# Kernel tuning notes

Hardware: AMD Instinct MI355X
Metric: run time of the kernel (lower is better)

## Reference

```python
import jax, jax.numpy as jnp
import numpy as np

B, D, H = 65536, 64, 512  # batch, input_dim (even), hidden_dim; num_layers=4 -> 4 Linears


def setup_inputs() -> dict:
    key = jax.random.key(0)
    ks = jax.random.split(key, 10)
    s_in = 1.0 / np.sqrt(D)
    s_h = 1.0 / np.sqrt(H)
    return {
        "t": jnp.zeros((1,), jnp.float32),
        "x": jax.random.normal(ks[0], (B, D), jnp.float32),
        "W0": jax.random.uniform(ks[1], (D, H), jnp.float32, -s_in, s_in),
        "b0": jax.random.uniform(ks[2], (H,), jnp.float32, -s_in, s_in),
        "W1": jax.random.uniform(ks[3], (H, H), jnp.float32, -s_h, s_h),
        "b1": jax.random.uniform(ks[4], (H,), jnp.float32, -s_h, s_h),
        "W2": jax.random.uniform(ks[5], (H, H), jnp.float32, -s_h, s_h),
        "b2": jax.random.uniform(ks[6], (H,), jnp.float32, -s_h, s_h),
        "W3": jax.random.uniform(ks[7], (H, 1), jnp.float32, -s_h, s_h),
        "b3": jax.random.uniform(ks[8], (1,), jnp.float32, -s_h, s_h),
    }


def reference(t, x, W0, b0, W1, b1, W2, b2, W3, b3):
    # Hamiltonian MLP: Linear->Tanh x3, final Linear to scalar energy per sample.
    def hamiltonian_sum(xx):
        h = jnp.tanh(xx @ W0 + b0)
        h = jnp.tanh(h @ W1 + b1)
        h = jnp.tanh(h @ W2 + b2)
        return jnp.sum(h @ W3 + b3)

    gradH = jax.grad(hamiltonian_sum)(x)  # [B, D]
    n = D // 2
    # gradH @ J.T with symplectic J == concat(gradH_p, -gradH_q)
    return jnp.concatenate([gradH[:, n:], -gradH[:, :n]], axis=1)
```

## Files before the change

### kernel.cpp

```cpp
#include <hip/hip_runtime.h>
#include <hip/hip_bf16.h>

typedef unsigned short u16;
typedef short s16x8 __attribute__((ext_vector_type(8)));
typedef float f32x4 __attribute__((ext_vector_type(4)));

#define MFMA_BF16(a, b, c) __builtin_amdgcn_mfma_f32_16x16x32_bf16((a), (b), (c), 0, 0, 0)

static constexpr int D_IN   = 64;
static constexpr int H_DIM  = 512;
static constexpr int M_TILE = 64;
static constexpr int AST    = 520;
static constexpr int XST    = 72;

__device__ __forceinline__ u16 f2bf(float f) {
  unsigned u = __builtin_bit_cast(unsigned, f);
  u += 0x7fffu + ((u >> 16) & 1u);
  return (u16)(u >> 16);
}
__device__ __forceinline__ float bfb2f(unsigned bits16) {
  return __builtin_bit_cast(float, bits16 << 16);
}
__device__ __forceinline__ float fast_tanh(float x) {
  float e = __expf(2.0f * x);
  return 1.0f - 2.0f * __builtin_amdgcn_rcpf(e + 1.0f);
}

__global__ void prep_weights(const float* __restrict__ W0,
                             const float* __restrict__ W1,
                             const float* __restrict__ W2,
                             u16* __restrict__ ws) {
  u16* p0f = ws;
  u16* p0b = p0f + D_IN * H_DIM;
  u16* p1f = p0b + D_IN * H_DIM;
  u16* p1b = p1f + H_DIM * H_DIM;
  u16* p2f = p1b + H_DIM * H_DIM;
  u16* p2b = p2f + H_DIM * H_DIM;

  int t = blockIdx.x * 256 + threadIdx.x;
  int lane = t & 63;
  int kc   = (t >> 6) & 15;
  int ntg  = t >> 10;
  int ln = lane & 15, q = lane >> 4;
  int n = ntg * 16 + ln;
  int k = kc * 32 + q * 8;

  #pragma unroll
  for (int j = 0; j < 8; ++j) {
    p1f[t * 8 + j] = f2bf(W1[(k + j) * 512 + n]);
    p2f[t * 8 + j] = f2bf(W2[(k + j) * 512 + n]);
    p1b[t * 8 + j] = f2bf(W1[n * 512 + (k + j)]);
    p2b[t * 8 + j] = f2bf(W2[n * 512 + (k + j)]);
  }
  if (kc < 2) {
    int t0 = (ntg * 2 + kc) * 64 + lane;
    #pragma unroll
    for (int j = 0; j < 8; ++j)
      p0f[t0 * 8 + j] = f2bf(W0[(k + j) * 512 + n]);
  }
  if (ntg < 4) {
    int t0 = (ntg * 16 + kc) * 64 + lane;
    #pragma unroll
    for (int j = 0; j < 8; ++j)
      p0b[t0 * 8 + j] = f2bf(W0[n * 512 + (k + j)]);
  }
}

#define LOAD_B4(BP, KC, BB)                                                     \
  {                                                                             \
    const u16* _sr = (BP) + ((size_t)wave << 15) + ((KC) << 9) + lane * 8;      \
    _Pragma("unroll")                                                           \
    for (int s = 0; s < 4; ++s)                                                 \
      (BB)[s] = *(const s16x8*)(_sr + (s << 13));                               \
  }
#define BB_PROLOGUE3(BP)                                                        \
  { LOAD_B4(BP, 0, bb0); LOAD_B4(BP, 1, bb1); LOAD_B4(BP, 2, bb2); }

#define STEP3(KC, BB, BP)                                                       \
  {                                                                             \
    s16x8 a[4];                                                                 \
    _Pragma("unroll")                                                           \
    for (int mt = 0; mt < 4; ++mt)                                              \
      a[mt] = *(const s16x8*)(buf + (mt * 16 + ln) * AST + (KC) * 32 + q * 8);  \
    _Pragma("unroll")                                                           \
    for (int nt = 0; nt < 4; ++nt)                                              \
      _Pragma("unroll")                                                         \
      for (int mt = 0; mt < 4; ++mt)                                            \
        acc[mt][nt] = MFMA_BF16(a[mt], (BB)[nt], acc[mt][nt]);                  \
    if ((KC) + 3 < 16) LOAD_B4(BP, (KC) + 3, BB);                               \
  }

#define GEMM512_REG(BP)                                                         \
  {                                                                             \
    _Pragma("unroll") for (int mt = 0; mt < 4; ++mt)                            \
      _Pragma("unroll") for (int nt = 0; nt < 4; ++nt)                          \
        acc[mt][nt] = (f32x4){0.f, 0.f, 0.f, 0.f};                              \
    STEP3( 0, bb0, BP); STEP3( 1, bb1, BP); STEP3( 2, bb2, BP);                 \
    STEP3( 3, bb0, BP); STEP3( 4, bb1, BP); STEP3( 5, bb2, BP);                 \
    STEP3( 6, bb0, BP); STEP3( 7, bb1, BP); STEP3( 8, bb2, BP);                 \
    STEP3( 9, bb0, BP); STEP3(10, bb1, BP); STEP3(11, bb2, BP);                 \
    STEP3(12, bb0, BP); STEP3(13, bb1, BP); STEP3(14, bb2, BP);                 \
    STEP3(15, bb0, BP);                                                         \
  }

__global__ __launch_bounds__(512, 2) void hnn_fused(
    const float* __restrict__ x,
    const float* __restrict__ bias0,
    const float* __restrict__ bias1,
    const float* __restrict__ bias2,
    const float* __restrict__ W3,
    const u16* __restrict__ ws,
    float* __restrict__ out)
{
  const u16* p0f = ws;
  const u16* p0b = p0f + D_IN * H_DIM;
  const u16* p1f = p0b + D_IN * H_DIM;
  const u16* p1b = p1f + H_DIM * H_DIM;
  const u16* p2f = p1b + H_DIM * H_DIM;
  const u16* p2b = p2f + H_DIM * H_DIM;

  __shared__ __align__(16) u16 xs[M_TILE * XST];
  __shared__ __align__(16) u16 buf[M_TILE * AST];

  const int tid  = threadIdx.x;
  const int wave = tid >> 6;
  const int lane = tid & 63;
  const int ln   = lane & 15;
  const int q    = lane >> 4;
  const int nwb  = wave * 64;
  const int row0 = blockIdx.x * M_TILE;

  {
    int r = tid >> 3, c = (tid & 7) * 8;
    const float4* src = (const float4*)(x + (size_t)(row0 + r) * D_IN + c);
    float4 f0 = src[0];
    float4 f1 = src[1];
    u16* dst = xs + r * XST + c;
    dst[0] = f2bf(f0.x); dst[1] = f2bf(f0.y); dst[2] = f2bf(f0.z); dst[3] = f2bf(f0.w);
    dst[4] = f2bf(f1.x); dst[5] = f2bf(f1.y); dst[6] = f2bf(f1.z); dst[7] = f2bf(f1.w);
  }
  __syncthreads();

  f32x4 acc[4][4];
  s16x8 bb0[4], bb1[4], bb2[4];
  unsigned h0p[4][4][2];
  unsigned h1p[4][4][2];
  float bias[4];

  #pragma unroll
  for (int nt = 0; nt < 4; ++nt) bias[nt] = bias0[nwb + nt * 16 + ln];
  #pragma unroll
  for (int mt = 0; mt < 4; ++mt)
    #pragma unroll
    for (int nt = 0; nt < 4; ++nt) acc[mt][nt] = (f32x4){0.f, 0.f, 0.f, 0.f};
  {
    const u16* bpw0 = p0f + (wave << 12) + lane * 8;
    #pragma unroll
    for (int kc = 0; kc < 2; ++kc) {
      s16x8 a0[4];
      #pragma unroll
      for (int mt = 0; mt < 4; ++mt)
        a0[mt] = *(const s16x8*)(xs + (mt * 16 + ln) * XST + kc * 32 + q * 8);
      #pragma unroll
      for (int nt = 0; nt < 4; ++nt) {
        s16x8 b = *(const s16x8*)(bpw0 + (nt << 10) + (kc << 9));
        #pragma unroll
        for (int mt = 0; mt < 4; ++mt)
          acc[mt][nt] = MFMA_BF16(a0[mt], b, acc[mt][nt]);
      }
    }
  }
  BB_PROLOGUE3(p1f);
  #pragma unroll
  for (int mt = 0; mt < 4; ++mt)
    #pragma unroll
    for (int nt = 0; nt < 4; ++nt) {
      int col = nwb + nt * 16 + ln;
      u16 u[4];
      #pragma unroll
      for (int r = 0; r < 4; ++r) {
        float th = fast_tanh(acc[mt][nt][r] + bias[nt]);
        u[r] = f2bf(th);
        buf[(mt * 16 + q * 4 + r) * AST + col] = u[r];
      }
      h0p[mt][nt][0] = (unsigned)u[0] | ((unsigned)u[1] << 16);
      h0p[mt][nt][1] = (unsigned)u[2] | ((unsigned)u[3] << 16);
    }
  __syncthreads();

  #pragma unroll
  for (int nt = 0; nt < 4; ++nt) bias[nt] = bias1[nwb + nt * 16 + ln];
  GEMM512_REG(p1f);
  __syncthreads();
  BB_PROLOGUE3(p2f);
  #pragma unroll
  for (int mt = 0; mt < 4; ++mt)
    #pragma unroll
    for (int nt = 0; nt < 4; ++nt) {
      int col = nwb + nt * 16 + ln;
      u16 u[4];
      #pragma unroll
      for (int r = 0; r < 4; ++r) {
        float th = fast_tanh(acc[mt][nt][r] + bias[nt]);
        u[r] = f2bf(th);
        buf[(mt * 16 + q * 4 + r) * AST + col] = u[r];
      }
      h1p[mt][nt][0] = (unsigned)u[0] | ((unsigned)u[1] << 16);
      h1p[mt][nt][1] = (unsigned)u[2] | ((unsigned)u[3] << 16);
    }
  __syncthreads();

  #pragma unroll
  for (int nt = 0; nt < 4; ++nt) bias[nt] = bias2[nwb + nt * 16 + ln];
  float w3v[4];
  #pragma unroll
  for (int nt = 0; nt < 4; ++nt) w3v[nt] = W3[nwb + nt * 16 + ln];
  GEMM512_REG(p2f);
  __syncthreads();
  BB_PROLOGUE3(p2b);
  #pragma unroll
  for (int mt = 0; mt < 4; ++mt)
    #pragma unroll
    for (int nt = 0; nt < 4; ++nt) {
      int col = nwb + nt * 16 + ln;
      #pragma unroll
      for (int r = 0; r < 4; ++r) {
        float th = fast_tanh(acc[mt][nt][r] + bias[nt]);
        float gz = w3v[nt] * (1.0f - th * th);
        buf[(mt * 16 + q * 4 + r) * AST + col] = f2bf(gz);
      }
    }
  __syncthreads();

  GEMM512_REG(p2b);
  __syncthreads();
  BB_PROLOGUE3(p1b);
  #pragma unroll
  for (int mt = 0; mt < 4; ++mt)
    #pragma unroll
    for (int nt = 0; nt < 4; ++nt) {
      int col = nwb + nt * 16 + ln;
      unsigned pa = h1p[mt][nt][0], pb = h1p[mt][nt][1];
      float hh[4] = { bfb2f(pa & 0xffffu), bfb2f(pa >> 16),
                      bfb2f(pb & 0xffffu), bfb2f(pb >> 16) };
      #pragma unroll
      for (int r = 0; r < 4; ++r) {
        float gz = acc[mt][nt][r] * (1.0f - hh[r] * hh[r]);
        buf[(mt * 16 + q * 4 + r) * AST + col] = f2bf(gz);
      }
    }
  __syncthreads();

  GEMM512_REG(p1b);
  __syncthreads();
  #pragma unroll
  for (int mt = 0; mt < 4; ++mt)
    #pragma unroll
    for (int nt = 0; nt < 4; ++nt) {
      int col = nwb + nt * 16 + ln;
      unsigned pa = h0p[mt][nt][0], pb = h0p[mt][nt][1];
      float hh[4] = { bfb2f(pa & 0xffffu), bfb2f(pa >> 16),
                      bfb2f(pb & 0xffffu), bfb2f(pb >> 16) };
      #pragma unroll
      for (int r = 0; r < 4; ++r) {
        float gz = acc[mt][nt][r] * (1.0f - hh[r] * hh[r]);
        buf[(mt * 16 + q * 4 + r) * AST + col] = f2bf(gz);
      }
    }
  __syncthreads();

  {
    f32x4 acc5[2];
    acc5[0] = (f32x4){0.f, 0.f, 0.f, 0.f};
    acc5[1] = (f32x4){0.f, 0.f, 0.f, 0.f};
    const int mt5 = wave & 3;
    const int nb5 = (wave >> 2) * 32;
    const u16* bp5 = p0b + ((wave >> 2) << 14) + lane * 8;
    #pragma unroll 2
    for (int kc = 0; kc < 16; ++kc) {
      s16x8 a5 = *(const s16x8*)(buf + (mt5 * 16 + ln) * AST + kc * 32 + q * 8);
      #pragma unroll
      for (int nt = 0; nt < 2; ++nt) {
        s16x8 b = *(const s16x8*)(bp5 + (nt << 13) + (kc << 9));
        acc5[nt] = MFMA_BF16(a5, b, acc5[nt]);
      }
    }
    #pragma unroll
    for (int nt = 0; nt < 2; ++nt) {
      int g = nb5 + nt * 16 + ln;
      int c = (g < 32) ? g + 32 : g - 32;
      float s = (g < 32) ? -1.0f : 1.0f;
      #pragma unroll
      for (int r = 0; r < 4; ++r) {
        int grow = row0 + mt5 * 16 + q * 4 + r;
        out[(size_t)grow * 64 + c] = s * acc5[nt][r];
      }
    }
  }
}

extern "C" void kernel_launch(void* const* d_in, const int* in_sizes, int n_in,
                              void* d_out, int out_size, void* d_ws, size_t ws_size,
                              hipStream_t stream) {
  const float* x  = (const float*)d_in[1];
  const float* W0 = (const float*)d_in[2];
  const float* b0 = (const float*)d_in[3];
  const float* W1 = (const float*)d_in[4];
  const float* b1 = (const float*)d_in[5];
  const float* W2 = (const float*)d_in[6];
  const float* b2 = (const float*)d_in[7];
  const float* W3 = (const float*)d_in[8];
  u16* ws = (u16*)d_ws;
  float* out = (float*)d_out;

  prep_weights<<<128, 256, 0, stream>>>(W0, W1, W2, ws);
  hnn_fused<<<65536 / M_TILE, 512, 0, stream>>>(x, b0, b1, b2, W3, ws, out);
}
```

Before: 228.6 us.

## Transpose GEMM roles so weights are A operand, activations stored transposed

Swaps operand roles so each GEMM computes the transposed product (weights as the A operand in registers, activations read from LDS as B). Epilogues then write packed 4-element bf16 vectors instead of scalar u16 stores. Bias is folded into the accumulator init, W3 is folded into the backward W2 weights during prep, packed bf16 conversion is used on gfx950, and output is written as float4. The aim is to cut epilogue ALU work and the number of LDS and global store instructions, at the cost of a different LDS access pattern that may bank-conflict.

Result: slower. 264.0 us (+15.5%).

```diff
diff --git a/kernel.cpp b/kernel.cpp
--- a/kernel.cpp
+++ b/kernel.cpp
@@ -25,10 +25,22 @@
   float e = __expf(2.0f * x);
   return 1.0f - 2.0f * __builtin_amdgcn_rcpf(e + 1.0f);
 }
+#if defined(__gfx950__) && __has_builtin(__builtin_amdgcn_cvt_pk_bf16_f32)
+__device__ __forceinline__ unsigned pk2bf(float a, float b) {
+  typedef __bf16 bf16x2_t __attribute__((ext_vector_type(2)));
+  bf16x2_t v = __builtin_amdgcn_cvt_pk_bf16_f32(a, b);
+  return __builtin_bit_cast(unsigned, v);
+}
+#else
+__device__ __forceinline__ unsigned pk2bf(float a, float b) {
+  return (unsigned)f2bf(a) | ((unsigned)f2bf(b) << 16);
+}
+#endif
 
 __global__ void prep_weights(const float* __restrict__ W0,
                              const float* __restrict__ W1,
                              const float* __restrict__ W2,
+                             const float* __restrict__ W3,
                              u16* __restrict__ ws) {
   u16* p0f = ws;
   u16* p0b = p0f + D_IN * H_DIM;
@@ -50,7 +62,7 @@
     p1f[t * 8 + j] = f2bf(W1[(k + j) * 512 + n]);
     p2f[t * 8 + j] = f2bf(W2[(k + j) * 512 + n]);
     p1b[t * 8 + j] = f2bf(W1[n * 512 + (k + j)]);
-    p2b[t * 8 + j] = f2bf(W2[n * 512 + (k + j)]);
+    p2b[t * 8 + j] = f2bf(W2[n * 512 + (k + j)] * W3[k + j]);
   }
   if (kc < 2) {
     int t0 = (ntg * 2 + kc) * 64 + lane;
@@ -66,41 +78,55 @@
   }
 }
 
-#define LOAD_B4(BP, KC, BB)                                                     \
+#define LOAD_W4(BP, KC, WA)                                                     \
   {                                                                             \
     const u16* _sr = (BP) + ((size_t)wave << 15) + ((KC) << 9) + lane * 8;      \
     _Pragma("unroll")                                                           \
     for (int s = 0; s < 4; ++s)                                                 \
-      (BB)[s] = *(const s16x8*)(_sr + (s << 13));                               \
-  }
-#define BB_PROLOGUE3(BP)                                                        \
-  { LOAD_B4(BP, 0, bb0); LOAD_B4(BP, 1, bb1); LOAD_B4(BP, 2, bb2); }
-
-#define STEP3(KC, BB, BP)                                                       \
-  {                                                                             \
-    s16x8 a[4];                                                                 \
+      (WA)[s] = *(const s16x8*)(_sr + (s << 13));                               \
+  }
+#define WA_PROLOGUE3(BP)                                                        \
+  { LOAD_W4(BP, 0, wa0); LOAD_W4(BP, 1, wa1); LOAD_W4(BP, 2, wa2); }
+
+#define STEP3(KC, WA, BP)                                                       \
+  {                                                                             \
+    s16x8 b[4];                                                                 \
     _Pragma("unroll")                                                           \
-    for (int mt = 0; mt < 4; ++mt)                                              \
-      a[mt] = *(const s16x8*)(buf + (mt * 16 + ln) * AST + (KC) * 32 + q * 8);  \
+    for (int nt = 0; nt < 4; ++nt)                                              \
+      b[nt] = *(const s16x8*)(buf + (nt * 16 + ln) * AST + (KC) * 32 + q * 8);  \
     _Pragma("unroll")                                                           \
     for (int nt = 0; nt < 4; ++nt)                                              \
       _Pragma("unroll")                                                         \
       for (int mt = 0; mt < 4; ++mt)                                            \
-        acc[mt][nt] = MFMA_BF16(a[mt], (BB)[nt], acc[mt][nt]);                  \
-    if ((KC) + 3 < 16) LOAD_B4(BP, (KC) + 3, BB);                               \
+        acc[mt][nt] = MFMA_BF16((WA)[mt], b[nt], acc[mt][nt]);                  \
+    if ((KC) + 3 < 16) LOAD_W4(BP, (KC) + 3, WA);                               \
   }
 
 #define GEMM512_REG(BP)                                                         \
+  {                                                                             \
+    STEP3( 0, wa0, BP); STEP3( 1, wa1, BP); STEP3( 2, wa2, BP);                 \
+    STEP3( 3, wa0, BP); STEP3( 4, wa1, BP); STEP3( 5, wa2, BP);                 \
+    STEP3( 6, wa0, BP); STEP3( 7, wa1, BP); STEP3( 8, wa2, BP);                 \
+    STEP3( 9, wa0, BP); STEP3(10, wa1, BP); STEP3(11, wa2, BP);                 \
+    STEP3(12, wa0, BP); STEP3(13, wa1, BP); STEP3(14, wa2, BP);                 \
+    STEP3(15, wa0, BP);                                                         \
+  }
+
+#define ACC_INIT_BIAS(BIAS)                                                     \
+  {                                                                             \
+    _Pragma("unroll")                                                           \
+    for (int mt = 0; mt < 4; ++mt) {                                            \
+      float4 bv = *(const float4*)((BIAS) + wave * 64 + mt * 16 + q * 4);       \
+      _Pragma("unroll")                                                         \
+      for (int nt = 0; nt < 4; ++nt)                                            \
+        acc[mt][nt] = (f32x4){bv.x, bv.y, bv.z, bv.w};                          \
+    }                                                                           \
+  }
+#define ACC_INIT_ZERO()                                                         \
   {                                                                             \
     _Pragma("unroll") for (int mt = 0; mt < 4; ++mt)                            \
       _Pragma("unroll") for (int nt = 0; nt < 4; ++nt)                          \
         acc[mt][nt] = (f32x4){0.f, 0.f, 0.f, 0.f};                              \
-    STEP3( 0, bb0, BP); STEP3( 1, bb1, BP); STEP3( 2, bb2, BP);                 \
-    STEP3( 3, bb0, BP); STEP3( 4, bb1, BP); STEP3( 5, bb2, BP);                 \
-    STEP3( 6, bb0, BP); STEP3( 7, bb1, BP); STEP3( 8, bb2, BP);                 \
-    STEP3( 9, bb0, BP); STEP3(10, bb1, BP); STEP3(11, bb2, BP);                 \
-    STEP3(12, bb0, BP); STEP3(13, bb1, BP); STEP3(14, bb2, BP);                 \
-    STEP3(15, bb0, BP);                                                         \
   }
 
 __global__ __launch_bounds__(512, 2) void hnn_fused(
@@ -108,7 +134,6 @@
     const float* __restrict__ bias0,
     const float* __restrict__ bias1,
     const float* __restrict__ bias2,
-    const float* __restrict__ W3,
     const u16* __restrict__ ws,
     float* __restrict__ out)
 {
@@ -127,7 +152,7 @@
   const int lane = tid & 63;
   const int ln   = lane & 15;
   const int q    = lane >> 4;
-  const int nwb  = wave * 64;
+  const int m0   = wave * 64;
   const int row0 = blockIdx.x * M_TILE;
 
   {
@@ -142,130 +167,110 @@
   __syncthreads();
 
   f32x4 acc[4][4];
-  s16x8 bb0[4], bb1[4], bb2[4];
+  s16x8 wa0[4], wa1[4], wa2[4];
   unsigned h0p[4][4][2];
   unsigned h1p[4][4][2];
-  float bias[4];
-
-  #pragma unroll
-  for (int nt = 0; nt < 4; ++nt) bias[nt] = bias0[nwb + nt * 16 + ln];
-  #pragma unroll
-  for (int mt = 0; mt < 4; ++mt)
-    #pragma unroll
-    for (int nt = 0; nt < 4; ++nt) acc[mt][nt] = (f32x4){0.f, 0.f, 0.f, 0.f};
+
+  ACC_INIT_BIAS(bias0);
   {
-    const u16* bpw0 = p0f + (wave << 12) + lane * 8;
+    const u16* ap0 = p0f + (wave << 12) + lane * 8;
     #pragma unroll
     for (int kc = 0; kc < 2; ++kc) {
-      s16x8 a0[4];
+      s16x8 b[4];
       #pragma unroll
-      for (int mt = 0; mt < 4; ++mt)
-        a0[mt] = *(const s16x8*)(xs + (mt * 16 + ln) * XST + kc * 32 + q * 8);
+      for (int nt = 0; nt < 4; ++nt)
+        b[nt] = *(const s16x8*)(xs + (nt * 16 + ln) * XST + kc * 32 + q * 8);
       #pragma unroll
-      for (int nt = 0; nt < 4; ++nt) {
-        s16x8 b = *(const s16x8*)(bpw0 + (nt << 10) + (kc << 9));
+      for (int mt = 0; mt < 4; ++mt) {
+        s16x8 a = *(const s16x8*)(ap0 + (mt << 10) + (kc << 9));
         #pragma unroll
-        for (int mt = 0; mt < 4; ++mt)
-          acc[mt][nt] = MFMA_BF16(a0[mt], b, acc[mt][nt]);
+        for (int nt = 0; nt < 4; ++nt)
+          acc[mt][nt] = MFMA_BF16(a, b[nt], acc[mt][nt]);
       }
     }
   }
-  BB_PROLOGUE3(p1f);
-  #pragma unroll
-  for (int mt = 0; mt < 4; ++mt)
-    #pragma unroll
-    for (int nt = 0; nt < 4; ++nt) {
-      int col = nwb + nt * 16 + ln;
-      u16 u[4];
-      #pragma unroll
-      for (int r = 0; r < 4; ++r) {
-        float th = fast_tanh(acc[mt][nt][r] + bias[nt]);
-        u[r] = f2bf(th);
-        buf[(mt * 16 + q * 4 + r) * AST + col] = u[r];
-      }
-      h0p[mt][nt][0] = (unsigned)u[0] | ((unsigned)u[1] << 16);
-      h0p[mt][nt][1] = (unsigned)u[2] | ((unsigned)u[3] << 16);
-    }
-  __syncthreads();
-
-  #pragma unroll
-  for (int nt = 0; nt < 4; ++nt) bias[nt] = bias1[nwb + nt * 16 + ln];
+  WA_PROLOGUE3(p1f);
+  #pragma unroll
+  for (int mt = 0; mt < 4; ++mt)
+    #pragma unroll
+    for (int nt = 0; nt < 4; ++nt) {
+      unsigned p01 = pk2bf(fast_tanh(acc[mt][nt][0]), fast_tanh(acc[mt][nt][1]));
+      unsigned p23 = pk2bf(fast_tanh(acc[mt][nt][2]), fast_tanh(acc[mt][nt][3]));
+      h0p[mt][nt][0] = p01; h0p[mt][nt][1] = p23;
+      *(uint2*)(buf + (nt * 16 + ln) * AST + m0 + mt * 16 + q * 4) =
+          make_uint2(p01, p23);
+    }
+  __syncthreads();
+
+  ACC_INIT_BIAS(bias1);
   GEMM512_REG(p1f);
   __syncthreads();
-  BB_PROLOGUE3(p2f);
-  #pragma unroll
-  for (int mt = 0; mt < 4; ++mt)
-    #pragma unroll
-    for (int nt = 0; nt < 4; ++nt) {
-      int col = nwb + nt * 16 + ln;
-      u16 u[4];
-      #pragma unroll
-      for (int r = 0; r < 4; ++r) {
-        float th = fast_tanh(acc[mt][nt][r] + bias[nt]);
-        u[r] = f2bf(th);
-        buf[(mt * 16 + q * 4 + r) * AST + col] = u[r];
-      }
-      h1p[mt][nt][0] = (unsigned)u[0] | ((unsigned)u[1] << 16);
-      h1p[mt][nt][1] = (unsigned)u[2] | ((unsigned)u[3] << 16);
-    }
-  __syncthreads();
-
-  #pragma unroll
-  for (int nt = 0; nt < 4; ++nt) bias[nt] = bias2[nwb + nt * 16 + ln];
-  float w3v[4];
-  #pragma unroll
-  for (int nt = 0; nt < 4; ++nt) w3v[nt] = W3[nwb + nt * 16 + ln];
+  WA_PROLOGUE3(p2f);
+  #pragma unroll
+  for (int mt = 0; mt < 4; ++mt)
+    #pragma unroll
+    for (int nt = 0; nt < 4; ++nt) {
+      unsigned p01 = pk2bf(fast_tanh(acc[mt][nt][0]), fast_tanh(acc[mt][nt][1]));
+      unsigned p23 = pk2bf(fast_tanh(acc[mt][nt][2]), fast_tanh(acc[mt][nt][3]));
+      h1p[mt][nt][0] = p01; h1p[mt][nt][1] = p23;
+      *(uint2*)(buf + (nt * 16 + ln) * AST + m0 + mt * 16 + q * 4) =
+          make_uint2(p01, p23);
+    }
+  __syncthreads();
+
+  ACC_INIT_BIAS(bias2);
   GEMM512_REG(p2f);
   __syncthreads();
-  BB_PROLOGUE3(p2b);
-  #pragma unroll
-  for (int mt = 0; mt < 4; ++mt)
-    #pragma unroll
-    for (int nt = 0; nt < 4; ++nt) {
-      int col = nwb + nt * 16 + ln;
-      #pragma unroll
-      for (int r = 0; r < 4; ++r) {
-        float th = fast_tanh(acc[mt][nt][r] + bias[nt]);
-        float gz = w3v[nt] * (1.0f - th * th);
-        buf[(mt * 16 + q * 4 + r) * AST + col] = f2bf(gz);
-      }
-    }
-  __syncthreads();
-
+  WA_PROLOGUE3(p2b);
+  #pragma unroll
+  for (int mt = 0; mt < 4; ++mt)
+    #pragma unroll
+    for (int nt = 0; nt < 4; ++nt) {
+      float t0 = fast_tanh(acc[mt][nt][0]), t1 = fast_tanh(acc[mt][nt][1]);
+      float t2 = fast_tanh(acc[mt][nt][2]), t3 = fast_tanh(acc[mt][nt][3]);
+      unsigned p01 = pk2bf(1.0f - t0 * t0, 1.0f - t1 * t1);
+      unsigned p23 = pk2bf(1.0f - t2 * t2, 1.0f - t3 * t3);
+      *(uint2*)(buf + (nt * 16 + ln) * AST + m0 + mt * 16 + q * 4) =
+          make_uint2(p01, p23);
+    }
+  __syncthreads();
+
+  ACC_INIT_ZERO();
   GEMM512_REG(p2b);
   __syncthreads();
-  BB_PROLOGUE3(p1b);
-  #pragma unroll
-  for (int mt = 0; mt < 4; ++mt)
-    #pragma unroll
-    for (int nt = 0; nt < 4; ++nt) {
-      int col = nwb + nt * 16 + ln;
+  WA_PROLOGUE3(p1b);
+  #pragma unroll
+  for (int mt = 0; mt < 4; ++mt)
+    #pragma unroll
+    for (int nt = 0; nt < 4; ++nt) {
       unsigned pa = h1p[mt][nt][0], pb = h1p[mt][nt][1];
-      float hh[4] = { bfb2f(pa & 0xffffu), bfb2f(pa >> 16),
-                      bfb2f(pb & 0xffffu), bfb2f(pb >> 16) };
-      #pragma unroll
-      for (int r = 0; r < 4; ++r) {
-        float gz = acc[mt][nt][r] * (1.0f - hh[r] * hh[r]);
-        buf[(mt * 16 + q * 4 + r) * AST + col] = f2bf(gz);
-      }
-    }
-  __syncthreads();
-
+      float h0v = bfb2f(pa & 0xffffu), h1v = bfb2f(pa >> 16);
+      float h2v = bfb2f(pb & 0xffffu), h3v = bfb2f(pb >> 16);
+      unsigned p01 = pk2bf(acc[mt][nt][0] * (1.0f - h0v * h0v),
+                           acc[mt][nt][1] * (1.0f - h1v * h1v));
+      unsigned p23 = pk2bf(acc[mt][nt][2] * (1.0f - h2v * h2v),
+                           acc[mt][nt][3] * (1.0f - h3v * h3v));
+      *(uint2*)(buf + (nt * 16 + ln) * AST + m0 + mt * 16 + q * 4) =
+          make_uint2(p01, p23);
+    }
+  __syncthreads();
+
+  ACC_INIT_ZERO();
   GEMM512_REG(p1b);
   __syncthreads();
   #pragma unroll
   for (int mt = 0; mt < 4; ++mt)
     #pragma unroll
     for (int nt = 0; nt < 4; ++nt) {
-      int col = nwb + nt * 16 + ln;
       unsigned pa = h0p[mt][nt][0], pb = h0p[mt][nt][1];
-      float hh[4] = { bfb2f(pa & 0xffffu), bfb2f(pa >> 16),
-                      bfb2f(pb & 0xffffu), bfb2f(pb >> 16) };
-      #pragma unroll
-      for (int r = 0; r < 4; ++r) {
-        float gz = acc[mt][nt][r] * (1.0f - hh[r] * hh[r]);
-        buf[(mt * 16 + q * 4 + r) * AST + col] = f2bf(gz);
-      }
+      float h0v = bfb2f(pa & 0xffffu), h1v = bfb2f(pa >> 16);
+      float h2v = bfb2f(pb & 0xffffu), h3v = bfb2f(pb >> 16);
+      unsigned p01 = pk2bf(acc[mt][nt][0] * (1.0f - h0v * h0v),
+                           acc[mt][nt][1] * (1.0f - h1v * h1v));
+      unsigned p23 = pk2bf(acc[mt][nt][2] * (1.0f - h2v * h2v),
+                           acc[mt][nt][3] * (1.0f - h3v * h3v));
+      *(uint2*)(buf + (nt * 16 + ln) * AST + m0 + mt * 16 + q * 4) =
+          make_uint2(p01, p23);
     }
   __syncthreads();
 
@@ -274,27 +279,26 @@
     acc5[0] = (f32x4){0.f, 0.f, 0.f, 0.f};
     acc5[1] = (f32x4){0.f, 0.f, 0.f, 0.f};
     const int mt5 = wave & 3;
-    const int nb5 = (wave >> 2) * 32;
-    const u16* bp5 = p0b + ((wave >> 2) << 14) + lane * 8;
+    const int n0  = (wave >> 2) * 32;
+    const u16* ap5 = p0b + (mt5 << 13) + lane * 8;
     #pragma unroll 2
     for (int kc = 0; kc < 16; ++kc) {
-      s16x8 a5 = *(const s16x8*)(buf + (mt5 * 16 + ln) * AST + kc * 32 + q * 8);
+      s16x8 a = *(const s16x8*)(ap5 + (kc << 9));
       #pragma unroll
       for (int nt = 0; nt < 2; ++nt) {
-        s16x8 b = *(const s16x8*)(bp5 + (nt << 13) + (kc << 9));
-        acc5[nt] = MFMA_BF16(a5, b, acc5[nt]);
+        s16x8 b = *(const s16x8*)(buf + (n0 + nt * 16 + ln) * AST + kc * 32 + q * 8);
+        acc5[nt] = MFMA_BF16(a, b, acc5[nt]);
       }
     }
+    int g0 = mt5 * 16 + q * 4;
+    int c0 = (g0 < 32) ? g0 + 32 : g0 - 32;
+    float s = (g0 < 32) ? -1.0f : 1.0f;
     #pragma unroll
     for (int nt = 0; nt < 2; ++nt) {
-      int g = nb5 + nt * 16 + ln;
-      int c = (g < 32) ? g + 32 : g - 32;
-      float s = (g < 32) ? -1.0f : 1.0f;
-      #pragma unroll
-      for (int r = 0; r < 4; ++r) {
-        int grow = row0 + mt5 * 16 + q * 4 + r;
-        out[(size_t)grow * 64 + c] = s * acc5[nt][r];
-      }
+      int smp = row0 + n0 + nt * 16 + ln;
+      float4 v = make_float4(s * acc5[nt][0], s * acc5[nt][1],
+                             s * acc5[nt][2], s * acc5[nt][3]);
+      *(float4*)(out + (size_t)smp * 64 + c0) = v;
     }
   }
 }
@@ -313,6 +317,6 @@
   u16* ws = (u16*)d_ws;
   float* out = (float*)d_out;
 
-  prep_weights<<<128, 256, 0, stream>>>(W0, W1, W2, ws);
-  hnn_fused<<<65536 / M_TILE, 512, 0, stream>>>(x, b0, b1, b2, W3, ws, out);
-}
+  prep_weights<<<128, 256, 0, stream>>>(W0, W1, W2, W3, ws);
+  hnn_fused<<<65536 / M_TILE, 512, 0, stream>>>(x, b0, b1, b2, ws, out);
+}
```
